# Kernel optimization log

Measured on AMD Instinct MI355X. Metric: run time of the kernel, lower is better.

Reference implementation:

```python
import jax, jax.numpy as jnp
import numpy as np

N = 50000      # total packed nodes
E = 1600000    # edges (no self loops; layers add them)
G = 64         # graphs in the batch
F_IN = 24      # raw node feature dim
D = 64         # hidden dim
H = 4          # attention heads
C = D // H     # 16 channels per head
L = 3          # GAT layers
NEG = 0.2      # LeakyReLU negative slope (GATv2 default)
EPS = 1e-5     # LayerNorm eps


def setup_inputs() -> dict:
    key = jax.random.key(0)
    ks = jax.random.split(key, 16)
    x = jax.random.normal(ks[0], (N, F_IN), jnp.float32)
    src = jax.random.randint(ks[1], (E,), 0, N)
    dst = jax.random.randint(ks[2], (E,), 0, N)
    dst = jnp.where(dst == src, (dst + 1) % N, dst)  # keep edge list self-loop free
    edge_index = jnp.stack([src, dst]).astype(jnp.int32)
    batch = jnp.sort(jax.random.randint(ks[3], (N,), 0, G)).astype(jnp.int32)
    s = 0.1
    return dict(
        x=x, edge_index=edge_index, batch=batch,
        w_in=jax.random.normal(ks[4], (F_IN, D), jnp.float32) * s,
        b_in=jnp.zeros((D,), jnp.float32),
        w_l=jax.random.normal(ks[5], (L, D, D), jnp.float32) * s,
        b_l=jnp.zeros((L, D), jnp.float32),
        w_r=jax.random.normal(ks[6], (L, D, D), jnp.float32) * s,
        b_r=jnp.zeros((L, D), jnp.float32),
        att=jax.random.normal(ks[7], (L, H, C), jnp.float32) * s,
        b_gat=jnp.zeros((L, D), jnp.float32),
        ln_g=jnp.ones((L, D), jnp.float32),
        ln_b=jnp.zeros((L, D), jnp.float32),
        w_g1=jax.random.normal(ks[8], (D, D // 2), jnp.float32) * s,
        b_g1=jnp.zeros((D // 2,), jnp.float32),
        w_g2=jax.random.normal(ks[9], (D // 2, 1), jnp.float32) * s,
        b_g2=jnp.zeros((1,), jnp.float32),
        w_out=jax.random.normal(ks[10], (D, D), jnp.float32) * s,
        b_out=jnp.zeros((D,), jnp.float32),
    )


def _layernorm(h, g, b):
    m = h.mean(-1, keepdims=True)
    v = ((h - m) ** 2).mean(-1, keepdims=True)
    return (h - m) * jax.lax.rsqrt(v + EPS) * g + b


def _gatv2(h, src, dst, wl, bl, wr, br, att, bg):
    n = h.shape[0]
    xl = (h @ wl + bl).reshape(n, H, C)   # source transform
    xr = (h @ wr + br).reshape(n, H, C)   # target transform
    # edge scores: att . leaky_relu(xl[j] + xr[i])  -> [E', H]
    e = jnp.sum(jax.nn.leaky_relu(xl[src] + xr[dst], NEG) * att, axis=-1)
    emax = jax.ops.segment_max(e, dst, num_segments=n)
    ex = jnp.exp(e - emax[dst])
    denom = jax.ops.segment_sum(ex, dst, num_segments=n)
    alpha = ex / denom[dst]               # segment softmax over incoming edges
    out = jax.ops.segment_sum(alpha[:, :, None] * xl[src], dst, num_segments=n)
    return out.reshape(n, D) + bg


def reference(x, edge_index, batch, w_in, b_in, w_l, b_l, w_r, b_r, att, b_gat,
              ln_g, ln_b, w_g1, b_g1, w_g2, b_g2, w_out, b_out):
    n = x.shape[0]
    loops = jnp.arange(n, dtype=edge_index.dtype)
    src = jnp.concatenate([edge_index[0], loops])  # add self loops once
    dst = jnp.concatenate([edge_index[1], loops])
    h = jax.nn.relu(x @ w_in + b_in)
    for i in range(L):
        res = h
        h = _gatv2(h, src, dst, w_l[i], b_l[i], w_r[i], b_r[i], att[i], b_gat[i])
        h = _layernorm(h + res, ln_g[i], ln_b[i])
        if i < L - 1:
            h = jax.nn.relu(h)
    # GlobalAttention pooling: gate MLP -> per-graph softmax -> weighted sum
    gate = jax.nn.relu(h @ w_g1 + b_g1) @ w_g2 + b_g2  # [N, 1]
    gmax = jax.ops.segment_max(gate, batch, num_segments=G)
    ge = jnp.exp(gate - gmax[batch])
    gs = jax.ops.segment_sum(ge, batch, num_segments=G)
    a = ge / jnp.where(gs > 0, gs, 1.0)[batch]
    emb = jax.ops.segment_sum(a * h, batch, num_segments=G)  # [G, D]
    return jax.nn.relu(emb @ w_out + b_out)
```

## Files before the change

kernel.cpp:

```cpp
#include <hip/hip_runtime.h>

#define NEGS   0.2f
#define LN_EPS 1e-5f
#define BSH    7
#define BN     128
#define TILE   4096
#define LOG2E  1.44269504f

typedef const float* __restrict__ fp;
typedef _Float16 v2h __attribute__((ext_vector_type(2)));
typedef _Float16 v8h __attribute__((ext_vector_type(8)));
typedef float    v4f __attribute__((ext_vector_type(4)));

__device__ __forceinline__ v2h u2h(unsigned u){ union{unsigned u; v2h h;} c; c.u = u; return c.h; }
__device__ __forceinline__ unsigned h2u(v2h h){ union{v2h h; unsigned u;} c; c.h = h; return c.u; }

template<int CTRL>
__device__ __forceinline__ float dppadd(float x){
  int y = __builtin_amdgcn_update_dpp(0, __float_as_int(x), CTRL, 0xF, 0xF, true);
  return x + __int_as_float(y);
}
__device__ __forceinline__ float hsum8(float s){
  s = dppadd<0xB1>(s);
  s = dppadd<0x4E>(s);
  s = dppadd<0x141>(s);
  return s;
}

__device__ __forceinline__ float dot8(v8h a, v8h b, float init){
  union U { v8h v; v2h h[4]; };
  U ua; ua.v = a;
  U ub; ub.v = b;
  float s = init;
  #pragma unroll
  for (int i = 0; i < 4; ++i) s = __builtin_amdgcn_fdot2(ua.h[i], ub.h[i], s, false);
  return s;
}

__device__ __forceinline__ v8h leaky8(v8h t){
  return __builtin_elementwise_max(t, t * (_Float16)NEGS);
}

__device__ __forceinline__ float edge_w8(v8h v, v8h xr8, v8h att8, float negm2){
  v8h t = leaky8(v + xr8);
  float s = dppadd<0xB1>(dot8(t, att8, negm2));
  return __builtin_amdgcn_exp2f(s);
}

__global__ __launch_bounds__(256) void k_in(fp x, fp w, fp b, float* __restrict__ h,
                                            unsigned* __restrict__ h16, int N){
  __shared__ float ws[24*64];
  __shared__ float bs[64];
  __shared__ float xs[4][24];
  int tid = threadIdx.x;
  for (int i = tid; i < 24*64; i += 256) ws[i] = w[i];
  if (tid < 64) bs[tid] = b[tid];
  int r = tid >> 6, c = tid & 63;
  int row = blockIdx.x*4 + r;
  if (c < 24 && row < N) xs[r][c] = x[row*24 + c];
  __syncthreads();
  float acc = bs[c];
  #pragma unroll
  for (int k = 0; k < 24; ++k) acc = fmaf(xs[r][k], ws[k*64 + c], acc);
  float y = fmaxf(acc, 0.f);
  float y1 = __shfl_down(y, 1);
  if (row < N){
    h[(size_t)row*64 + c] = y;
    if (!(c & 1)){
      v2h p; p.x = (_Float16)y; p.y = (_Float16)y1;
      h16[(size_t)row*32 + (c >> 1)] = h2u(p);
    }
  }
}

__global__ __launch_bounds__(256) void k_wprep(fp w_l, fp w_r, fp att, _Float16* __restrict__ wf,
                                               _Float16* __restrict__ att16){
  int lm = blockIdx.x;
  if (lm < 3){
    for (int d = threadIdx.x; d < 64; d += 256)
      att16[lm*64 + d] = (_Float16)(att[lm*64 + d] * LOG2E);
  }
  const float* src = ((lm & 1) ? w_r : w_l) + (lm >> 1)*4096;
  _Float16* dst = wf + lm*4096;
  for (int d = threadIdx.x; d < 4096; d += 256){
    int j = d & 7, l = (d >> 3) & 63, kc = (d >> 9) & 1, nt = d >> 10;
    int k = kc*32 + (l >> 4)*8 + j;
    int n = nt*16 + (l & 15);
    dst[d] = (_Float16)src[k*64 + n];
  }
}

__global__ __launch_bounds__(256) void t_hist(const int* __restrict__ dstA, int* __restrict__ counts,
                                              int E, int K, int ntiles){
  __shared__ int hist[512];
  int t = blockIdx.x, tid = threadIdx.x;
  for (int i = tid; i < K; i += 256) hist[i] = 0;
  __syncthreads();
  int e0 = t*TILE, e1 = min(e0 + TILE, E);
  for (int e = e0 + tid; e < e1; e += 256)
    atomicAdd(&hist[dstA[e] >> BSH], 1);
  __syncthreads();
  for (int i = tid; i < K; i += 256) counts[i*ntiles + t] = hist[i];
}

__global__ __launch_bounds__(512) void s_scan_tiles(int* __restrict__ counts, int* __restrict__ btotal,
                                                    int ntiles){
  __shared__ int s[512];
  int b = blockIdx.x, tid = threadIdx.x;
  int v = (tid < ntiles) ? counts[b*ntiles + tid] : 0;
  s[tid] = v;
  __syncthreads();
  for (int off = 1; off < 512; off <<= 1){
    int t = (tid >= off) ? s[tid - off] : 0;
    __syncthreads();
    s[tid] += t;
    __syncthreads();
  }
  if (tid < ntiles) counts[b*ntiles + tid] = s[tid] - v;
  if (tid == 511) btotal[b] = s[511];
}

__global__ __launch_bounds__(512) void s_scan_buckets(const int* __restrict__ btotal,
                                                      int* __restrict__ bbase, int K, int E){
  __shared__ int s[512];
  int tid = threadIdx.x;
  int v = (tid < K) ? btotal[tid] : 0;
  s[tid] = v;
  __syncthreads();
  for (int off = 1; off < 512; off <<= 1){
    int t = (tid >= off) ? s[tid - off] : 0;
    __syncthreads();
    s[tid] += t;
    __syncthreads();
  }
  if (tid < K) bbase[tid] = s[tid] - v;
  if (tid == 0) bbase[K] = E;
}

__global__ __launch_bounds__(256) void t_scatter(const int* __restrict__ srcA, const int* __restrict__ dstA,
                                                 const int* __restrict__ counts, const int* __restrict__ bbase,
                                                 unsigned* __restrict__ packed, int E, int K, int ntiles){
  __shared__ int gb[512];
  __shared__ int cur[512];
  int t = blockIdx.x, tid = threadIdx.x;
  for (int i = tid; i < K; i += 256){
    gb[i] = bbase[i] + counts[i*ntiles + t];
    cur[i] = 0;
  }
  __syncthreads();
  int e0 = t*TILE, e1 = min(e0 + TILE, E);
  for (int e = e0 + tid; e < e1; e += 256){
    int d = dstA[e], sv = srcA[e];
    int b = d >> BSH;
    int p = atomicAdd(&cur[b], 1);
    packed[gb[b] + p] = ((unsigned)(d & (BN-1)) << 25) | (unsigned)sv;
  }
}

__global__ __launch_bounds__(256) void k_fine(const unsigned* __restrict__ packed, const int* __restrict__ bbase,
                                              int* __restrict__ row_ptr, int* __restrict__ col, int N, int K){
  __shared__ int hist[BN];
  __shared__ int excl[BN];
  int b = blockIdx.x, tid = threadIdx.x;
  int node0 = b << BSH;
  int e_base = bbase[b], e_end = bbase[b+1];
  if (tid < BN) hist[tid] = 0;
  __syncthreads();
  for (int e = e_base + tid; e < e_end; e += 256)
    atomicAdd(&hist[packed[e] >> 25], 1);
  __syncthreads();
  int v = (tid < BN) ? hist[tid] : 0;
  if (tid < BN) excl[tid] = v;
  __syncthreads();
  for (int off = 1; off < BN; off <<= 1){
    int t2 = 0;
    if (tid < BN && tid >= off) t2 = excl[tid - off];
    __syncthreads();
    if (tid < BN) excl[tid] += t2;
    __syncthreads();
  }
  int nn = min(BN, N - node0);
  if (tid < nn) row_ptr[node0 + tid] = e_base + excl[tid] - v;
  if (b == K-1 && tid == 0) row_ptr[N] = e_end;
  if (tid < BN) hist[tid] = excl[tid] - v;
  __syncthreads();
  for (int e = e_base + tid; e < e_end; e += 256){
    unsigned u = packed[e];
    int dl = u >> 25;
    int p = atomicAdd(&hist[dl], 1);
    col[e_base + p] = (int)(u & 0x1FFFFFFu);
  }
}

__global__ __launch_bounds__(256) void k_xfm(const unsigned* __restrict__ h16,
                                             const _Float16* __restrict__ wf,
                                             fp blg, fp brg,
                                             unsigned* __restrict__ xl16, unsigned* __restrict__ xr16, int N){
  int tid = threadIdx.x, wave = tid >> 6, lane = tid & 63;
  int quad = lane >> 4, ln = lane & 15;
  int m0 = blockIdx.x*64 + wave*16;
  if (m0 >= N) return;
  int m = m0 + ln;
  bool mv = m < N;
  v8h a0 = {}, a1 = {};
  if (mv){
    a0 = *(const v8h*)&h16[(size_t)m*32 + quad*4];
    a1 = *(const v8h*)&h16[(size_t)m*32 + 16 + quad*4];
  }
  #pragma unroll
  for (int mat = 0; mat < 2; ++mat){
    const _Float16* wb = wf + mat*4096;
    fp bias = mat ? brg : blg;
    unsigned* dst = mat ? xr16 : xl16;
    #pragma unroll
    for (int nt = 0; nt < 4; ++nt){
      v8h b0 = *(const v8h*)&wb[nt*1024 + lane*8];
      v8h b1 = *(const v8h*)&wb[nt*1024 + 512 + lane*8];
      float bv = bias[nt*16 + ln];
      v4f acc = {bv, bv, bv, bv};
      acc = __builtin_amdgcn_mfma_f32_16x16x32_f16(a0, b0, acc, 0, 0, 0);
      acc = __builtin_amdgcn_mfma_f32_16x16x32_f16(a1, b1, acc, 0, 0, 0);
      #pragma unroll
      for (int r = 0; r < 4; ++r){
        float partner = __shfl_xor(acc[r], 1);
        int node = m0 + quad*4 + r;
        if (!(lane & 1) && node < N){
          v2h p; p.x = (_Float16)acc[r]; p.y = (_Float16)partner;
          dst[(size_t)node*32 + nt*8 + (ln >> 1)] = h2u(p);
        }
      }
    }
  }
}

__global__ __launch_bounds__(256) void k_gat(const unsigned* __restrict__ xl16, const unsigned* __restrict__ xr16,
                                             float* __restrict__ h, unsigned* __restrict__ h16,
                                             const int* __restrict__ row_ptr, const int* __restrict__ col,
                                             const _Float16* __restrict__ att16, fp bg, fp lng, fp lnb,
                                             int N, int do_relu){
  int lane = threadIdx.x & 63;
  int g = lane >> 3;
  int s = lane & 7;
  int node = (blockIdx.x*4 + (threadIdx.x >> 6))*8 + g;
  bool valid = node < N;
  int nodec = valid ? node : N - 1;

  v8h att8 = *(const v8h*)&att16[s*8];
  v8h xr8  = *(const v8h*)&xr16[(size_t)nodec*32 + s*4];
  v8h xl8  = *(const v8h*)&xl16[(size_t)nodec*32 + s*4];

  float m = dppadd<0xB1>(dot8(leaky8(xl8 + xr8), att8, 0.f));
  float negm2 = m * -0.5f;

  float den = 1.f;
  float acc[8];
  #pragma unroll
  for (int i = 0; i < 8; ++i) acc[i] = (float)xl8[i];

  int e  = row_ptr[nodec];
  int e1 = valid ? row_ptr[nodec + 1] : e;

  for (; e + 2 <= e1; e += 2){
    int j0 = col[e], j1 = col[e+1];
    v8h v0 = *(const v8h*)&xl16[(size_t)j0*32 + s*4];
    v8h v1 = *(const v8h*)&xl16[(size_t)j1*32 + s*4];
    float w0 = edge_w8(v0, xr8, att8, negm2);
    float w1 = edge_w8(v1, xr8, att8, negm2);
    den += w0 + w1;
    #pragma unroll
    for (int i = 0; i < 8; ++i){
      acc[i] = fmaf(w0, (float)v0[i], acc[i]);
      acc[i] = fmaf(w1, (float)v1[i], acc[i]);
    }
  }
  if (e < e1){
    int j0 = col[e];
    v8h v0 = *(const v8h*)&xl16[(size_t)j0*32 + s*4];
    float w0 = edge_w8(v0, xr8, att8, negm2);
    den += w0;
    #pragma unroll
    for (int i = 0; i < 8; ++i) acc[i] = fmaf(w0, (float)v0[i], acc[i]);
  }

  float inv = 1.f / den;

  float4 bgA = *(const float4*)&bg[s*8];
  float4 bgB = *(const float4*)&bg[s*8 + 4];
  float4 hA  = *(const float4*)&h[(size_t)nodec*64 + s*8];
  float4 hB  = *(const float4*)&h[(size_t)nodec*64 + s*8 + 4];
  float res8[8] = {hA.x + bgA.x, hA.y + bgA.y, hA.z + bgA.z, hA.w + bgA.w,
                   hB.x + bgB.x, hB.y + bgB.y, hB.z + bgB.z, hB.w + bgB.w};
  float o8[8];
  float sl = 0.f;
  #pragma unroll
  for (int i = 0; i < 8; ++i){ o8[i] = fmaf(acc[i], inv, res8[i]); sl += o8[i]; }
  sl = hsum8(sl);
  float mean = sl * (1.f/64.f);
  float vsl = 0.f;
  #pragma unroll
  for (int i = 0; i < 8; ++i){ o8[i] -= mean; vsl = fmaf(o8[i], o8[i], vsl); }
  vsl = hsum8(vsl);
  float rs = rsqrtf(vsl * (1.f/64.f) + LN_EPS);

  if (valid){
    float4 lgA = *(const float4*)&lng[s*8], lgB = *(const float4*)&lng[s*8 + 4];
    float4 lbA = *(const float4*)&lnb[s*8], lbB = *(const float4*)&lnb[s*8 + 4];
    float lg8[8] = {lgA.x, lgA.y, lgA.z, lgA.w, lgB.x, lgB.y, lgB.z, lgB.w};
    float lb8[8] = {lbA.x, lbA.y, lbA.z, lbA.w, lbB.x, lbB.y, lbB.z, lbB.w};
    float y[8];
    #pragma unroll
    for (int i = 0; i < 8; ++i){
      y[i] = fmaf(o8[i]*rs, lg8[i], lb8[i]);
      if (do_relu) y[i] = fmaxf(y[i], 0.f);
    }
    float4 yA = {y[0], y[1], y[2], y[3]};
    float4 yB = {y[4], y[5], y[6], y[7]};
    *(float4*)&h[(size_t)node*64 + s*8]     = yA;
    *(float4*)&h[(size_t)node*64 + s*8 + 4] = yB;
    v8h p;
    #pragma unroll
    for (int i = 0; i < 8; ++i) p[i] = (_Float16)y[i];
    *(v8h*)&h16[(size_t)node*32 + s*4] = p;
  }
}

__global__ __launch_bounds__(256) void k_gate(const float* __restrict__ h, fp w1, fp b1, fp w2, fp b2,
                                              float* __restrict__ gate, int N){
  __shared__ float w1s[2048];
  __shared__ float hrow[16][64];
  int tid = threadIdx.x;
  for (int i = tid*4; i < 2048; i += 1024) *(float4*)&w1s[i] = *(const float4*)&w1[i];
  int base = blockIdx.x*16;
  int nrows = min(16, N - base);
  int lim = nrows*64;
  for (int i = tid*4; i < lim; i += 1024)
    *(float4*)&hrow[0][i] = *(const float4*)&h[(size_t)base*64 + i];
  __syncthreads();
  int wave = tid >> 6, lane = tid & 63;
  int j = lane & 31, half = lane >> 5;
  float b1v = b1[j], w2v = w2[j], b2v = b2[0];
  int k0 = half*32;
  #pragma unroll
  for (int it = 0; it < 4; ++it){
    int r = wave*4 + it;
    int node = base + r;
    if (node >= N) break;
    float s = 0.f;
    #pragma unroll 8
    for (int k = k0; k < k0 + 32; ++k) s = fmaf(hrow[r][k], w1s[k*32 + j], s);
    s += __shfl_xor(s, 32);
    float hid = fmaxf(s + b1v, 0.f);
    float contrib = (half == 0) ? hid * w2v : 0.f;
    #pragma unroll
    for (int o = 1; o < 64; o <<= 1) contrib += __shfl_xor(contrib, o);
    if (lane == 0) gate[node] = contrib + b2v;
  }
}

__global__ __launch_bounds__(256) void k_gmax(const float* __restrict__ gate, const int* __restrict__ batch,
                                              float* __restrict__ gmax, float* __restrict__ gsum,
                                              float* __restrict__ embsum, int N){
  int g = blockIdx.x, tid = threadIdx.x;
  if (tid < 64) embsum[g*64 + tid] = 0.f;
  if (tid == 64) gsum[g] = 0.f;
  int lo = 0, hi = N;
  while (lo < hi){ int mid = (lo + hi) >> 1; if (batch[mid] < g) lo = mid + 1; else hi = mid; }
  int start = lo;
  hi = N;
  while (lo < hi){ int mid = (lo + hi) >> 1; if (batch[mid] < g + 1) lo = mid + 1; else hi = mid; }
  int end = lo;
  float m = -3.4e38f;
  for (int i = start + tid; i < end; i += 256) m = fmaxf(m, gate[i]);
  #pragma unroll
  for (int o = 1; o < 64; o <<= 1) m = fmaxf(m, __shfl_xor(m, o));
  __shared__ float ws[4];
  if ((tid & 63) == 0) ws[tid >> 6] = m;
  __syncthreads();
  if (tid == 0) gmax[g] = fmaxf(fmaxf(ws[0], ws[1]), fmaxf(ws[2], ws[3]));
}

__global__ __launch_bounds__(256) void k_emb(const float* __restrict__ h, const float* __restrict__ gate,
                                             const int* __restrict__ batch, const float* __restrict__ gmax,
                                             float* __restrict__ gsum, float* __restrict__ embsum, int N){
  int lane = threadIdx.x & 63;
  int wv = blockIdx.x*4 + (threadIdx.x >> 6);
  int s = wv*16;
  if (s >= N) return;
  int e = min(s + 16, N);
  int cur = batch[s];
  float gm = gmax[cur];
  float acc = 0.f, asum = 0.f;
  for (int i = s; i < e; ++i){
    int g = batch[i];
    if (g != cur){
      atomicAdd(&embsum[cur*64 + lane], acc);
      if (lane == 0) atomicAdd(&gsum[cur], asum);
      acc = 0.f; asum = 0.f; cur = g; gm = gmax[g];
    }
    float a = __expf(gate[i] - gm);
    acc = fmaf(a, h[(size_t)i*64 + lane], acc);
    asum += a;
  }
  atomicAdd(&embsum[cur*64 + lane], acc);
  if (lane == 0) atomicAdd(&gsum[cur], asum);
}

__global__ __launch_bounds__(64) void k_out(const float* __restrict__ embsum, const float* __restrict__ gsum,
                                            fp w_out, fp b_out, float* __restrict__ out, int G){
  int g = blockIdx.x, lane = threadIdx.x;
  __shared__ float emb[64];
  float gs = gsum[g];
  float inv = (gs > 0.f) ? 1.f/gs : 1.f;
  emb[lane] = embsum[g*64 + lane] * inv;
  __syncthreads();
  float o2 = b_out[lane];
  #pragma unroll 8
  for (int d = 0; d < 64; ++d) o2 = fmaf(emb[d], w_out[d*64 + lane], o2);
  out[g*64 + lane] = fmaxf(o2, 0.f);
}

extern "C" void kernel_launch(void* const* d_in, const int* in_sizes, int n_in,
                              void* d_out, int out_size, void* d_ws, size_t ws_size,
                              hipStream_t stream) {
  const int N = in_sizes[0] / 24;
  const int E = in_sizes[1] / 2;
  const int G = out_size / 64;
  const int K = (N + BN - 1) >> BSH;
  const int ntiles = (E + TILE - 1) / TILE;

  fp x      = (fp)d_in[0];
  const int* edge  = (const int*)d_in[1];
  const int* batch = (const int*)d_in[2];
  fp w_in   = (fp)d_in[3];
  fp b_in   = (fp)d_in[4];
  fp w_l    = (fp)d_in[5];
  fp b_l    = (fp)d_in[6];
  fp w_r    = (fp)d_in[7];
  fp b_r    = (fp)d_in[8];
  fp att    = (fp)d_in[9];
  fp b_gat  = (fp)d_in[10];
  fp ln_g   = (fp)d_in[11];
  fp ln_b   = (fp)d_in[12];
  fp w_g1   = (fp)d_in[13];
  fp b_g1   = (fp)d_in[14];
  fp w_g2   = (fp)d_in[15];
  fp b_g2   = (fp)d_in[16];
  fp w_out  = (fp)d_in[17];
  fp b_out  = (fp)d_in[18];
  float* out = (float*)d_out;

  char* wp = (char*)d_ws;
  auto alloc = [&](size_t bytes) -> char* {
    char* p = wp; wp += (bytes + 255) & ~(size_t)255; return p;
  };
  float*    h       = (float*)    alloc((size_t)N*64*sizeof(float));
  unsigned* h16     = (unsigned*) alloc((size_t)N*32*sizeof(unsigned));
  unsigned* xl16    = (unsigned*) alloc((size_t)N*32*sizeof(unsigned));
  unsigned* xr16    = (unsigned*) alloc((size_t)N*32*sizeof(unsigned));
  int*      col     = (int*)      alloc((size_t)E*sizeof(int));
  unsigned* packed  = (unsigned*) alloc((size_t)E*sizeof(unsigned));
  int*      counts  = (int*)      alloc((size_t)K*ntiles*sizeof(int));
  int*      btotal  = (int*)      alloc((size_t)K*sizeof(int));
  int*      bbase   = (int*)      alloc((size_t)(K+1)*sizeof(int));
  int*      row_ptr = (int*)      alloc((size_t)(N+1)*sizeof(int));
  float*    gate    = (float*)    alloc((size_t)N*sizeof(float));
  float*    gmax    = (float*)    alloc((size_t)G*sizeof(float));
  float*    gsum    = (float*)    alloc((size_t)(G + G*64)*sizeof(float));
  float*    embsum  = gsum + G;
  _Float16* wf      = (_Float16*) alloc((size_t)3*2*4096*sizeof(_Float16));
  _Float16* att16g  = (_Float16*) alloc((size_t)3*64*sizeof(_Float16));

  const int* srcA = edge;
  const int* dstA = edge + E;

  k_in<<<(N + 3)/4, 256, 0, stream>>>(x, w_in, b_in, h, h16, N);
  k_wprep<<<6, 256, 0, stream>>>(w_l, w_r, att, wf, att16g);

  t_hist<<<ntiles, 256, 0, stream>>>(dstA, counts, E, K, ntiles);
  s_scan_tiles<<<K, 512, 0, stream>>>(counts, btotal, ntiles);
  s_scan_buckets<<<1, 512, 0, stream>>>(btotal, bbase, K, E);
  t_scatter<<<ntiles, 256, 0, stream>>>(srcA, dstA, counts, bbase, packed, E, K, ntiles);
  k_fine<<<K, 256, 0, stream>>>(packed, bbase, row_ptr, col, N, K);

  for (int i = 0; i < 3; ++i){
    k_xfm<<<(N + 63)/64, 256, 0, stream>>>(h16, wf + i*8192, b_l + i*64, b_r + i*64,
                                           xl16, xr16, N);
    k_gat<<<(N + 31)/32, 256, 0, stream>>>(xl16, xr16, h, h16, row_ptr, col,
                                           att16g + i*64, b_gat + i*64, ln_g + i*64, ln_b + i*64,
                                           N, i < 2 ? 1 : 0);
  }
  k_gate<<<(N + 15)/16, 256, 0, stream>>>(h, w_g1, b_g1, w_g2, b_g2, gate, N);
  k_gmax<<<G, 256, 0, stream>>>(gate, batch, gmax, gsum, embsum, N);
  k_emb<<<(N + 255)/64, 256, 0, stream>>>(h, gate, batch, gmax, gsum, embsum, N);
  k_out<<<G, 64, 0, stream>>>(embsum, gsum, w_out, b_out, out, G);
}
```

Measured before the change: 344.9 us.

## Merge CSR build and pooling tail into cooperative kernels with grid syncs

```diff
diff --git a/kernel.cpp b/kernel.cpp
--- a/kernel.cpp
+++ b/kernel.cpp
@@ -1,4 +1,7 @@
 #include <hip/hip_runtime.h>
+#include <hip/hip_cooperative_groups.h>
+
+namespace cg = cooperative_groups;
 
 #define NEGS   0.2f
 #define LN_EPS 1e-5f
@@ -47,16 +50,35 @@
   return __builtin_amdgcn_exp2f(s);
 }
 
-__global__ __launch_bounds__(256) void k_in(fp x, fp w, fp b, float* __restrict__ h,
-                                            unsigned* __restrict__ h16, int N){
+__global__ __launch_bounds__(256) void k_setup(fp x, fp w, fp b, float* __restrict__ h,
+                                               unsigned* __restrict__ h16, int N,
+                                               fp w_l, fp w_r, fp att,
+                                               _Float16* __restrict__ wf, _Float16* __restrict__ att16){
   __shared__ float ws[24*64];
   __shared__ float bs[64];
   __shared__ float xs[4][24];
+  if (blockIdx.x < 6){
+    int lm = blockIdx.x;
+    if (lm < 3){
+      for (int d = threadIdx.x; d < 64; d += 256)
+        att16[lm*64 + d] = (_Float16)(att[lm*64 + d] * LOG2E);
+    }
+    const float* src = ((lm & 1) ? w_r : w_l) + (lm >> 1)*4096;
+    _Float16* dst = wf + lm*4096;
+    for (int d = threadIdx.x; d < 4096; d += 256){
+      int jj = d & 7, l = (d >> 3) & 63, kc = (d >> 9) & 1, nt = d >> 10;
+      int k = kc*32 + (l >> 4)*8 + jj;
+      int n = nt*16 + (l & 15);
+      dst[d] = (_Float16)src[k*64 + n];
+    }
+    return;
+  }
+  int blk = blockIdx.x - 6;
   int tid = threadIdx.x;
   for (int i = tid; i < 24*64; i += 256) ws[i] = w[i];
   if (tid < 64) bs[tid] = b[tid];
   int r = tid >> 6, c = tid & 63;
-  int row = blockIdx.x*4 + r;
+  int row = blk*4 + r;
   if (c < 24 && row < N) xs[r][c] = x[row*24 + c];
   __syncthreads();
   float acc = bs[c];
@@ -73,122 +95,106 @@
   }
 }
 
-__global__ __launch_bounds__(256) void k_wprep(fp w_l, fp w_r, fp att, _Float16* __restrict__ wf,
-                                               _Float16* __restrict__ att16){
-  int lm = blockIdx.x;
-  if (lm < 3){
-    for (int d = threadIdx.x; d < 64; d += 256)
-      att16[lm*64 + d] = (_Float16)(att[lm*64 + d] * LOG2E);
-  }
-  const float* src = ((lm & 1) ? w_r : w_l) + (lm >> 1)*4096;
-  _Float16* dst = wf + lm*4096;
-  for (int d = threadIdx.x; d < 4096; d += 256){
-    int j = d & 7, l = (d >> 3) & 63, kc = (d >> 9) & 1, nt = d >> 10;
-    int k = kc*32 + (l >> 4)*8 + j;
-    int n = nt*16 + (l & 15);
-    dst[d] = (_Float16)src[k*64 + n];
-  }
-}
-
-__global__ __launch_bounds__(256) void t_hist(const int* __restrict__ dstA, int* __restrict__ counts,
-                                              int E, int K, int ntiles){
-  __shared__ int hist[512];
-  int t = blockIdx.x, tid = threadIdx.x;
-  for (int i = tid; i < K; i += 256) hist[i] = 0;
-  __syncthreads();
-  int e0 = t*TILE, e1 = min(e0 + TILE, E);
-  for (int e = e0 + tid; e < e1; e += 256)
-    atomicAdd(&hist[dstA[e] >> BSH], 1);
-  __syncthreads();
-  for (int i = tid; i < K; i += 256) counts[i*ntiles + t] = hist[i];
-}
-
-__global__ __launch_bounds__(512) void s_scan_tiles(int* __restrict__ counts, int* __restrict__ btotal,
-                                                    int ntiles){
-  __shared__ int s[512];
-  int b = blockIdx.x, tid = threadIdx.x;
-  int v = (tid < ntiles) ? counts[b*ntiles + tid] : 0;
-  s[tid] = v;
-  __syncthreads();
-  for (int off = 1; off < 512; off <<= 1){
-    int t = (tid >= off) ? s[tid - off] : 0;
-    __syncthreads();
-    s[tid] += t;
-    __syncthreads();
-  }
-  if (tid < ntiles) counts[b*ntiles + tid] = s[tid] - v;
-  if (tid == 511) btotal[b] = s[511];
-}
-
-__global__ __launch_bounds__(512) void s_scan_buckets(const int* __restrict__ btotal,
-                                                      int* __restrict__ bbase, int K, int E){
-  __shared__ int s[512];
+__global__ __launch_bounds__(512) void k_csr(const int* __restrict__ srcA, const int* __restrict__ dstA,
+                                             int* __restrict__ counts, int* __restrict__ btotal,
+                                             int* __restrict__ bbase, unsigned* __restrict__ packed,
+                                             int* __restrict__ row_ptr, int* __restrict__ col,
+                                             int E, int N, int K, int ntiles){
+  cg::grid_group grid = cg::this_grid();
+  __shared__ int sm[1024];
   int tid = threadIdx.x;
-  int v = (tid < K) ? btotal[tid] : 0;
-  s[tid] = v;
-  __syncthreads();
-  for (int off = 1; off < 512; off <<= 1){
-    int t = (tid >= off) ? s[tid - off] : 0;
-    __syncthreads();
-    s[tid] += t;
-    __syncthreads();
-  }
-  if (tid < K) bbase[tid] = s[tid] - v;
-  if (tid == 0) bbase[K] = E;
-}
-
-__global__ __launch_bounds__(256) void t_scatter(const int* __restrict__ srcA, const int* __restrict__ dstA,
-                                                 const int* __restrict__ counts, const int* __restrict__ bbase,
-                                                 unsigned* __restrict__ packed, int E, int K, int ntiles){
-  __shared__ int gb[512];
-  __shared__ int cur[512];
-  int t = blockIdx.x, tid = threadIdx.x;
-  for (int i = tid; i < K; i += 256){
-    gb[i] = bbase[i] + counts[i*ntiles + t];
-    cur[i] = 0;
-  }
-  __syncthreads();
-  int e0 = t*TILE, e1 = min(e0 + TILE, E);
-  for (int e = e0 + tid; e < e1; e += 256){
-    int d = dstA[e], sv = srcA[e];
-    int b = d >> BSH;
-    int p = atomicAdd(&cur[b], 1);
-    packed[gb[b] + p] = ((unsigned)(d & (BN-1)) << 25) | (unsigned)sv;
-  }
-}
-
-__global__ __launch_bounds__(256) void k_fine(const unsigned* __restrict__ packed, const int* __restrict__ bbase,
-                                              int* __restrict__ row_ptr, int* __restrict__ col, int N, int K){
-  __shared__ int hist[BN];
-  __shared__ int excl[BN];
-  int b = blockIdx.x, tid = threadIdx.x;
-  int node0 = b << BSH;
-  int e_base = bbase[b], e_end = bbase[b+1];
-  if (tid < BN) hist[tid] = 0;
-  __syncthreads();
-  for (int e = e_base + tid; e < e_end; e += 256)
-    atomicAdd(&hist[packed[e] >> 25], 1);
-  __syncthreads();
-  int v = (tid < BN) ? hist[tid] : 0;
-  if (tid < BN) excl[tid] = v;
-  __syncthreads();
-  for (int off = 1; off < BN; off <<= 1){
-    int t2 = 0;
-    if (tid < BN && tid >= off) t2 = excl[tid - off];
-    __syncthreads();
-    if (tid < BN) excl[tid] += t2;
-    __syncthreads();
-  }
-  int nn = min(BN, N - node0);
-  if (tid < nn) row_ptr[node0 + tid] = e_base + excl[tid] - v;
-  if (b == K-1 && tid == 0) row_ptr[N] = e_end;
-  if (tid < BN) hist[tid] = excl[tid] - v;
-  __syncthreads();
-  for (int e = e_base + tid; e < e_end; e += 256){
-    unsigned u = packed[e];
-    int dl = u >> 25;
-    int p = atomicAdd(&hist[dl], 1);
-    col[e_base + p] = (int)(u & 0x1FFFFFFu);
+  int b = blockIdx.x;
+
+  if (b < ntiles){
+    for (int i = tid; i < K; i += 512) sm[i] = 0;
+    __syncthreads();
+    int e0 = b*TILE, e1 = min(e0 + TILE, E);
+    for (int e = e0 + tid; e < e1; e += 512)
+      atomicAdd(&sm[dstA[e] >> BSH], 1);
+    __syncthreads();
+    for (int i = tid; i < K; i += 512) counts[i*ntiles + b] = sm[i];
+  }
+  grid.sync();
+
+  if (b < K){
+    int v = (tid < ntiles) ? counts[b*ntiles + tid] : 0;
+    sm[tid] = v;
+    __syncthreads();
+    for (int off = 1; off < 512; off <<= 1){
+      int t = (tid >= off) ? sm[tid - off] : 0;
+      __syncthreads();
+      sm[tid] += t;
+      __syncthreads();
+    }
+    if (tid < ntiles) counts[b*ntiles + tid] = sm[tid] - v;
+    if (tid == 511) btotal[b] = sm[511];
+  }
+  grid.sync();
+
+  if (b == 0){
+    int v = (tid < K) ? btotal[tid] : 0;
+    sm[tid] = v;
+    __syncthreads();
+    for (int off = 1; off < 512; off <<= 1){
+      int t = (tid >= off) ? sm[tid - off] : 0;
+      __syncthreads();
+      sm[tid] += t;
+      __syncthreads();
+    }
+    if (tid < K) bbase[tid] = sm[tid] - v;
+    if (tid == 0) bbase[K] = E;
+  }
+  grid.sync();
+
+  if (b < ntiles){
+    int* gb  = sm;
+    int* cur = sm + 512;
+    for (int i = tid; i < K; i += 512){
+      gb[i] = bbase[i] + counts[i*ntiles + b];
+      cur[i] = 0;
+    }
+    __syncthreads();
+    int e0 = b*TILE, e1 = min(e0 + TILE, E);
+    for (int e = e0 + tid; e < e1; e += 512){
+      int d = dstA[e], sv = srcA[e];
+      int bk = d >> BSH;
+      int p = atomicAdd(&cur[bk], 1);
+      packed[gb[bk] + p] = ((unsigned)(d & (BN-1)) << 25) | (unsigned)sv;
+    }
+  }
+  grid.sync();
+
+  if (b < K){
+    int* hist = sm;
+    int* excl = sm + 512;
+    int node0 = b << BSH;
+    int e_base = bbase[b], e_end = bbase[b+1];
+    if (tid < BN) hist[tid] = 0;
+    __syncthreads();
+    for (int e = e_base + tid; e < e_end; e += 512)
+      atomicAdd(&hist[packed[e] >> 25], 1);
+    __syncthreads();
+    int v = (tid < BN) ? hist[tid] : 0;
+    if (tid < BN) excl[tid] = v;
+    __syncthreads();
+    for (int off = 1; off < BN; off <<= 1){
+      int t2 = 0;
+      if (tid < BN && tid >= off) t2 = excl[tid - off];
+      __syncthreads();
+      if (tid < BN) excl[tid] += t2;
+      __syncthreads();
+    }
+    int nn = min(BN, N - node0);
+    if (tid < nn) row_ptr[node0 + tid] = e_base + excl[tid] - v;
+    if (b == K-1 && tid == 0) row_ptr[N] = e_end;
+    if (tid < BN) hist[tid] = excl[tid] - v;
+    __syncthreads();
+    for (int e = e_base + tid; e < e_end; e += 512){
+      unsigned u = packed[e];
+      int dl = u >> 25;
+      int p = atomicAdd(&hist[dl], 1);
+      col[e_base + p] = (int)(u & 0x1FFFFFFu);
+    }
   }
 }
 
@@ -324,99 +330,107 @@
   }
 }
 
-__global__ __launch_bounds__(256) void k_gate(const float* __restrict__ h, fp w1, fp b1, fp w2, fp b2,
-                                              float* __restrict__ gate, int N){
+__global__ __launch_bounds__(256) void k_tail(const float* __restrict__ h, fp w1, fp b1, fp w2, fp b2,
+                                              const int* __restrict__ batch, fp w_out, fp b_out,
+                                              float* __restrict__ gate, float* __restrict__ gmax,
+                                              float* __restrict__ gsum, float* __restrict__ embsum,
+                                              float* __restrict__ out, int N, int G){
+  cg::grid_group grid = cg::this_grid();
   __shared__ float w1s[2048];
   __shared__ float hrow[16][64];
+  __shared__ float ws4[4];
+  __shared__ float embs[64];
   int tid = threadIdx.x;
+  int wave = tid >> 6, lane = tid & 63;
+
   for (int i = tid*4; i < 2048; i += 1024) *(float4*)&w1s[i] = *(const float4*)&w1[i];
-  int base = blockIdx.x*16;
-  int nrows = min(16, N - base);
-  int lim = nrows*64;
-  for (int i = tid*4; i < lim; i += 1024)
-    *(float4*)&hrow[0][i] = *(const float4*)&h[(size_t)base*64 + i];
-  __syncthreads();
-  int wave = tid >> 6, lane = tid & 63;
   int j = lane & 31, half = lane >> 5;
   float b1v = b1[j], w2v = w2[j], b2v = b2[0];
   int k0 = half*32;
-  #pragma unroll
-  for (int it = 0; it < 4; ++it){
-    int r = wave*4 + it;
-    int node = base + r;
-    if (node >= N) break;
-    float s = 0.f;
-    #pragma unroll 8
-    for (int k = k0; k < k0 + 32; ++k) s = fmaf(hrow[r][k], w1s[k*32 + j], s);
-    s += __shfl_xor(s, 32);
-    float hid = fmaxf(s + b1v, 0.f);
-    float contrib = (half == 0) ? hid * w2v : 0.f;
+  int nchunks = (N + 15)/16;
+  for (int c = blockIdx.x; c < nchunks; c += gridDim.x){
+    int base = c*16;
+    int nrows = min(16, N - base);
+    int lim = nrows*64;
+    __syncthreads();
+    for (int i = tid*4; i < lim; i += 1024)
+      *(float4*)&hrow[0][i] = *(const float4*)&h[(size_t)base*64 + i];
+    __syncthreads();
+    for (int it = 0; it < 4; ++it){
+      int r = wave*4 + it;
+      int node = base + r;
+      if (node >= N) break;
+      float s = 0.f;
+      #pragma unroll 8
+      for (int k = k0; k < k0 + 32; ++k) s = fmaf(hrow[r][k], w1s[k*32 + j], s);
+      s += __shfl_xor(s, 32);
+      float hid = fmaxf(s + b1v, 0.f);
+      float contrib = (half == 0) ? hid * w2v : 0.f;
+      #pragma unroll
+      for (int o = 1; o < 64; o <<= 1) contrib += __shfl_xor(contrib, o);
+      if (lane == 0) gate[node] = contrib + b2v;
+    }
+  }
+  grid.sync();
+
+  for (int g = blockIdx.x; g < G; g += gridDim.x){
+    if (tid < 64) embsum[g*64 + tid] = 0.f;
+    if (tid == 64) gsum[g] = 0.f;
+    int lo = 0, hi = N;
+    while (lo < hi){ int mid = (lo + hi) >> 1; if (batch[mid] < g) lo = mid + 1; else hi = mid; }
+    int start = lo;
+    hi = N;
+    while (lo < hi){ int mid = (lo + hi) >> 1; if (batch[mid] < g + 1) lo = mid + 1; else hi = mid; }
+    int end = lo;
+    float m = -3.4e38f;
+    for (int i = start + tid; i < end; i += 256) m = fmaxf(m, gate[i]);
     #pragma unroll
-    for (int o = 1; o < 64; o <<= 1) contrib += __shfl_xor(contrib, o);
-    if (lane == 0) gate[node] = contrib + b2v;
-  }
-}
-
-__global__ __launch_bounds__(256) void k_gmax(const float* __restrict__ gate, const int* __restrict__ batch,
-                                              float* __restrict__ gmax, float* __restrict__ gsum,
-                                              float* __restrict__ embsum, int N){
-  int g = blockIdx.x, tid = threadIdx.x;
-  if (tid < 64) embsum[g*64 + tid] = 0.f;
-  if (tid == 64) gsum[g] = 0.f;
-  int lo = 0, hi = N;
-  while (lo < hi){ int mid = (lo + hi) >> 1; if (batch[mid] < g) lo = mid + 1; else hi = mid; }
-  int start = lo;
-  hi = N;
-  while (lo < hi){ int mid = (lo + hi) >> 1; if (batch[mid] < g + 1) lo = mid + 1; else hi = mid; }
-  int end = lo;
-  float m = -3.4e38f;
-  for (int i = start + tid; i < end; i += 256) m = fmaxf(m, gate[i]);
-  #pragma unroll
-  for (int o = 1; o < 64; o <<= 1) m = fmaxf(m, __shfl_xor(m, o));
-  __shared__ float ws[4];
-  if ((tid & 63) == 0) ws[tid >> 6] = m;
-  __syncthreads();
-  if (tid == 0) gmax[g] = fmaxf(fmaxf(ws[0], ws[1]), fmaxf(ws[2], ws[3]));
-}
-
-__global__ __launch_bounds__(256) void k_emb(const float* __restrict__ h, const float* __restrict__ gate,
-                                             const int* __restrict__ batch, const float* __restrict__ gmax,
-                                             float* __restrict__ gsum, float* __restrict__ embsum, int N){
-  int lane = threadIdx.x & 63;
-  int wv = blockIdx.x*4 + (threadIdx.x >> 6);
-  int s = wv*16;
-  if (s >= N) return;
-  int e = min(s + 16, N);
-  int cur = batch[s];
-  float gm = gmax[cur];
-  float acc = 0.f, asum = 0.f;
-  for (int i = s; i < e; ++i){
-    int g = batch[i];
-    if (g != cur){
-      atomicAdd(&embsum[cur*64 + lane], acc);
-      if (lane == 0) atomicAdd(&gsum[cur], asum);
-      acc = 0.f; asum = 0.f; cur = g; gm = gmax[g];
-    }
-    float a = __expf(gate[i] - gm);
-    acc = fmaf(a, h[(size_t)i*64 + lane], acc);
-    asum += a;
-  }
-  atomicAdd(&embsum[cur*64 + lane], acc);
-  if (lane == 0) atomicAdd(&gsum[cur], asum);
-}
-
-__global__ __launch_bounds__(64) void k_out(const float* __restrict__ embsum, const float* __restrict__ gsum,
-                                            fp w_out, fp b_out, float* __restrict__ out, int G){
-  int g = blockIdx.x, lane = threadIdx.x;
-  __shared__ float emb[64];
-  float gs = gsum[g];
-  float inv = (gs > 0.f) ? 1.f/gs : 1.f;
-  emb[lane] = embsum[g*64 + lane] * inv;
-  __syncthreads();
-  float o2 = b_out[lane];
-  #pragma unroll 8
-  for (int d = 0; d < 64; ++d) o2 = fmaf(emb[d], w_out[d*64 + lane], o2);
-  out[g*64 + lane] = fmaxf(o2, 0.f);
+    for (int o = 1; o < 64; o <<= 1) m = fmaxf(m, __shfl_xor(m, o));
+    if ((tid & 63) == 0) ws4[tid >> 6] = m;
+    __syncthreads();
+    if (tid == 0) gmax[g] = fmaxf(fmaxf(ws4[0], ws4[1]), fmaxf(ws4[2], ws4[3]));
+    __syncthreads();
+  }
+  grid.sync();
+
+  int nwv = (N + 15)/16;
+  for (int wv = blockIdx.x*4 + wave; wv < nwv; wv += gridDim.x*4){
+    int s0 = wv*16;
+    int e = min(s0 + 16, N);
+    int cur = batch[s0];
+    float gm = gmax[cur];
+    float acc = 0.f, asum = 0.f;
+    for (int i = s0; i < e; ++i){
+      int g = batch[i];
+      if (g != cur){
+        atomicAdd(&embsum[cur*64 + lane], acc);
+        if (lane == 0) atomicAdd(&gsum[cur], asum);
+        acc = 0.f; asum = 0.f; cur = g; gm = gmax[g];
+      }
+      float a = __expf(gate[i] - gm);
+      acc = fmaf(a, h[(size_t)i*64 + lane], acc);
+      asum += a;
+    }
+    atomicAdd(&embsum[cur*64 + lane], acc);
+    if (lane == 0) atomicAdd(&gsum[cur], asum);
+  }
+  grid.sync();
+
+  for (int g = blockIdx.x; g < G; g += gridDim.x){
+    __syncthreads();
+    if (tid < 64){
+      float gs = gsum[g];
+      float inv = (gs > 0.f) ? 1.f/gs : 1.f;
+      embs[tid] = embsum[g*64 + tid] * inv;
+    }
+    __syncthreads();
+    if (tid < 64){
+      float o2 = b_out[tid];
+      #pragma unroll 8
+      for (int d = 0; d < 64; ++d) o2 = fmaf(embs[d], w_out[d*64 + tid], o2);
+      out[g*64 + tid] = fmaxf(o2, 0.f);
+    }
+  }
 }
 
 extern "C" void kernel_launch(void* const* d_in, const int* in_sizes, int n_in,
@@ -473,14 +487,15 @@
   const int* srcA = edge;
   const int* dstA = edge + E;
 
-  k_in<<<(N + 3)/4, 256, 0, stream>>>(x, w_in, b_in, h, h16, N);
-  k_wprep<<<6, 256, 0, stream>>>(w_l, w_r, att, wf, att16g);
-
-  t_hist<<<ntiles, 256, 0, stream>>>(dstA, counts, E, K, ntiles);
-  s_scan_tiles<<<K, 512, 0, stream>>>(counts, btotal, ntiles);
-  s_scan_buckets<<<1, 512, 0, stream>>>(btotal, bbase, K, E);
-  t_scatter<<<ntiles, 256, 0, stream>>>(srcA, dstA, counts, bbase, packed, E, K, ntiles);
-  k_fine<<<K, 256, 0, stream>>>(packed, bbase, row_ptr, col, N, K);
+  k_setup<<<(N + 3)/4 + 6, 256, 0, stream>>>(x, w_in, b_in, h, h16, N, w_l, w_r, att, wf, att16g);
+
+  {
+    int Em = E, Nm = N, Km = K, ntm = ntiles;
+    int gsz = (K > ntiles) ? K : ntiles;
+    void* args[] = { (void*)&srcA, (void*)&dstA, (void*)&counts, (void*)&btotal, (void*)&bbase,
+                     (void*)&packed, (void*)&row_ptr, (void*)&col, &Em, &Nm, &Km, &ntm };
+    hipLaunchCooperativeKernel((void*)k_csr, dim3(gsz), dim3(512), args, 0, stream);
+  }
 
   for (int i = 0; i < 3; ++i){
     k_xfm<<<(N + 63)/64, 256, 0, stream>>>(h16, wf + i*8192, b_l + i*64, b_r + i*64,
@@ -489,8 +504,13 @@
                                            att16g + i*64, b_gat + i*64, ln_g + i*64, ln_b + i*64,
                                            N, i < 2 ? 1 : 0);
   }
-  k_gate<<<(N + 15)/16, 256, 0, stream>>>(h, w_g1, b_g1, w_g2, b_g2, gate, N);
-  k_gmax<<<G, 256, 0, stream>>>(gate, batch, gmax, gsum, embsum, N);
-  k_emb<<<(N + 255)/64, 256, 0, stream>>>(h, gate, batch, gmax, gsum, embsum, N);
-  k_out<<<G, 64, 0, stream>>>(embsum, gsum, w_out, b_out, out, G);
-}
+
+  {
+    int Nm = N, Gm = G;
+    void* args[] = { (void*)&h, (void*)&w_g1, (void*)&b_g1, (void*)&w_g2, (void*)&b_g2,
+                     (void*)&batch, (void*)&w_out, (void*)&b_out,
+                     (void*)&gate, (void*)&gmax, (void*)&gsum, (void*)&embsum,
+                     (void*)&out, &Nm, &Gm };
+    hipLaunchCooperativeKernel((void*)k_tail, dim3(256), dim3(256), args, 0, stream);
+  }
+}
```

Result: slower. 675.1 us (+95.7%).
